# Kernel optimization log

Hardware: AMD Instinct MI355X
Metric: run time of the kernel (lower is better)

Reference implementation:

```python
import jax, jax.numpy as jnp
import numpy as np

CH = 512
RED = CH // 8  # 64


def setup_inputs() -> dict:
    key = jax.random.key(0)
    ks = jax.random.split(key, 8)
    s = 0.05
    x = jax.random.normal(ks[0], (4, CH, 64, 64), dtype=jnp.float32)
    Wq = jax.random.normal(ks[1], (RED, CH), dtype=jnp.float32) * s
    bq = jnp.zeros((RED,), dtype=jnp.float32)
    Wk = jax.random.normal(ks[2], (RED, CH), dtype=jnp.float32) * s
    bk = jnp.zeros((RED,), dtype=jnp.float32)
    Wv = jax.random.normal(ks[3], (CH, CH), dtype=jnp.float32) * s
    bv = jnp.zeros((CH,), dtype=jnp.float32)
    gamma = jnp.zeros((1,), dtype=jnp.float32)
    return {"x": x, "Wq": Wq, "bq": bq, "Wk": Wk, "bk": bk, "Wv": Wv, "bv": bv, "gamma": gamma}


def reference(x, Wq, bq, Wk, bk, Wv, bv, gamma):
    b, c, h, w = x.shape
    n = h * w
    xf = x.reshape(b, c, n)  # [b, c, n]
    # 1x1 convs == per-pixel linear over channels
    q = jnp.einsum('rc,bcn->bnr', Wq, xf) + bq[None, None, :]   # [b, n, red]
    k = jnp.einsum('rc,bcn->brn', Wk, xf) + bk[None, :, None]   # [b, red, n]
    v = jnp.einsum('oc,bcn->bon', Wv, xf) + bv[None, :, None]   # [b, c, n]
    energy = jnp.einsum('bnr,brm->bnm', q, k)                   # [b, n, n]
    attention = jax.nn.softmax(energy, axis=-1)
    # out[b,c,i] = sum_j v[b,c,j] * attention[b,i,j]
    out = jnp.einsum('bcj,bij->bci', v, attention).reshape(b, c, h, w)
    return gamma[0] * out + x
```

## Files before the change

kernel.cpp:

```cpp
#include <hip/hip_runtime.h>
#include <math.h>

#define CH 512
#define RED 64

typedef __attribute__((ext_vector_type(4))) float f32x4;
typedef long i64;

typedef const __attribute__((address_space(1))) void* gas_t;
typedef __attribute__((address_space(3))) void* las_t;

static __device__ __forceinline__ void gl16(const void* g, void* l) {
    __builtin_amdgcn_global_load_lds((gas_t)g, (las_t)l, 16, 0, 0);
}

static __device__ __forceinline__ unsigned pk4(float a, float b, float c, float d) {
    int w = __builtin_amdgcn_cvt_pk_fp8_f32(a, b, 0, false);
    w = __builtin_amdgcn_cvt_pk_fp8_f32(c, d, w, true);
    return (unsigned)w;
}
static __device__ __forceinline__ unsigned char pk1(float a) {
    return (unsigned char)(__builtin_amdgcn_cvt_pk_fp8_f32(a, a, 0, false) & 0xFF);
}

static __device__ __forceinline__ float fexp2(float v) {
#if __has_builtin(__builtin_amdgcn_exp2f)
    return __builtin_amdgcn_exp2f(v);
#else
    float r; asm("v_exp_f32 %0, %1" : "=v"(r) : "v"(v)); return r;
#endif
}

__global__ __launch_bounds__(128) void prep_w(
    const float* __restrict__ Wq, const float* __restrict__ Wk,
    const float* __restrict__ Wv, unsigned char* __restrict__ Wcat)
{
    const int r = blockIdx.x, t = threadIdx.x;
    const float* src = (r < 64) ? (Wq + (size_t)r * CH)
                     : (r < 128) ? (Wk + (size_t)(r - 64) * CH)
                                 : (Wv + (size_t)(r - 128) * CH);
    const float4 v = *(const float4*)&src[t * 4];
    *(unsigned*)&Wcat[(size_t)r * CH + t * 4] = pk4(v.x, v.y, v.z, v.w);
}

__global__ __launch_bounds__(256) void cast_xt(
    const float* __restrict__ x, unsigned char* __restrict__ xT, int n)
{
    __shared__ float sX[64][65];
    const int b = blockIdx.z, i0 = blockIdx.x * 64, c0 = blockIdx.y * 64;
    const int t = threadIdx.x;
    #pragma unroll
    for (int s = 0; s < 4; ++s) {
        const int id = s * 256 + t, c = id >> 4, seg = id & 15;
        *(float4*)&sX[c][seg * 4] = *(const float4*)&x[((size_t)b * CH + c0 + c) * n + i0 + seg * 4];
    }
    __syncthreads();
    const int i = t >> 2, cp = t & 3;
    uint4 w;
    w.x = pk4(sX[cp*16+ 0][i], sX[cp*16+ 1][i], sX[cp*16+ 2][i], sX[cp*16+ 3][i]);
    w.y = pk4(sX[cp*16+ 4][i], sX[cp*16+ 5][i], sX[cp*16+ 6][i], sX[cp*16+ 7][i]);
    w.z = pk4(sX[cp*16+ 8][i], sX[cp*16+ 9][i], sX[cp*16+10][i], sX[cp*16+11][i]);
    w.w = pk4(sX[cp*16+12][i], sX[cp*16+13][i], sX[cp*16+14][i], sX[cp*16+15][i]);
    *(uint4*)&xT[((size_t)b * n + i0 + i) * CH + c0 + cp * 16] = w;
}

__global__ __launch_bounds__(256, 4) void qkv_gemm(
    const unsigned char* __restrict__ xT, const unsigned char* __restrict__ Wcat,
    const float* __restrict__ bq, const float* __restrict__ bk,
    const float* __restrict__ bv,
    unsigned char* __restrict__ qF, unsigned char* __restrict__ kF,
    unsigned char* __restrict__ v2, int n)
{
    __shared__ char smem[20480];
    const int b = blockIdx.z, i0 = blockIdx.x * 128, o0 = blockIdx.y * 128;
    const int t = threadIdx.x, lane = t & 63;
    const int quad = lane >> 4, l16 = lane & 15;
    const int wrow = (t >> 6) & 1, wcol = t >> 7;

    f32x4 acc[4][4];
    const f32x4 zz = {0.f, 0.f, 0.f, 0.f};
    #pragma unroll
    for (int mi = 0; mi < 4; ++mi)
        #pragma unroll
        for (int ci = 0; ci < 4; ++ci) acc[mi][ci] = zz;

    const unsigned char* Ab = xT + ((size_t)b * n + i0) * CH;
    const unsigned char* Bb = Wcat + (size_t)o0 * CH;

    for (int c0 = 0; c0 < CH; c0 += 64) {
        #pragma unroll
        for (int s = 0; s < 5; ++s) {
            const int c = s * 256 + t;
            const bool isA = c < 640;
            const int tc = isA ? c : c - 640;
            const int r = tc / 5, p = (tc % 5) & 3;
            gl16((isA ? Ab : Bb) + (size_t)r * CH + c0 + p * 16,
                 smem + (isA ? 0 : 10240) + (size_t)tc * 16);
        }
        __syncthreads();
        #pragma unroll
        for (int kk = 0; kk < 64; kk += 32) {
            i64 af[4], bf[4];
            #pragma unroll
            for (int mi = 0; mi < 4; ++mi)
                af[mi] = *(const i64*)(smem + (wrow * 64 + mi * 16 + l16) * 80 + kk + quad * 8);
            #pragma unroll
            for (int ci = 0; ci < 4; ++ci)
                bf[ci] = *(const i64*)(smem + 10240 + (wcol * 64 + ci * 16 + l16) * 80 + kk + quad * 8);
            #pragma unroll
            for (int mi = 0; mi < 4; ++mi)
                #pragma unroll
                for (int ci = 0; ci < 4; ++ci)
                    acc[mi][ci] = __builtin_amdgcn_mfma_f32_16x16x32_fp8_fp8(af[mi], bf[ci], acc[mi][ci], 0, 0, 0);
        }
        __syncthreads();
    }

    float bb[4], scl[4];
    #pragma unroll
    for (int ci = 0; ci < 4; ++ci) {
        const int o = wcol * 64 + ci * 16 + l16;
        if (o0 == 0) {
            bb[ci]  = (o < 64) ? bq[o] : bk[o - 64];
            scl[ci] = (o < 64) ? 1.44269504088896f : 1.0f;
        } else {
            bb[ci]  = bv[o0 - 128 + o];
            scl[ci] = 1.0f;
        }
    }
    __syncthreads();
    unsigned char* sE = (unsigned char*)smem;
    if (o0 == 0) {
        #pragma unroll
        for (int mi = 0; mi < 4; ++mi)
            #pragma unroll
            for (int ci = 0; ci < 4; ++ci)
                #pragma unroll
                for (int r = 0; r < 4; ++r)
                    sE[(wrow*64 + mi*16 + quad*4 + r) * 144 + wcol*64 + ci*16 + l16] =
                        pk1((acc[mi][ci][r] + bb[ci]) * scl[ci]);
    } else {
        #pragma unroll
        for (int mi = 0; mi < 4; ++mi)
            #pragma unroll
            for (int ci = 0; ci < 4; ++ci)
                #pragma unroll
                for (int r = 0; r < 4; ++r)
                    sE[(wcol*64 + ci*16 + l16) * 144 + wrow*64 + mi*16 + quad*4 + r] =
                        pk1(acc[mi][ci][r] + bb[ci]);
    }
    __syncthreads();
    if (o0 == 0) {
        #pragma unroll
        for (int u = 0; u < 2; ++u) {
            const int id = u * 256 + t, i = id >> 2, p = id & 3;
            *(uint4*)&qF[((size_t)b * n + i0 + i) * RED + p * 16] = *(const uint4*)&sE[i * 144 + p * 16];
        }
        #pragma unroll
        for (int u = 0; u < 2; ++u) {
            const int id = u * 256 + t, i = id >> 2, p = id & 3;
            *(uint4*)&kF[((size_t)b * n + i0 + i) * RED + p * 16] = *(const uint4*)&sE[i * 144 + 64 + p * 16];
        }
    } else {
        #pragma unroll
        for (int u = 0; u < 4; ++u) {
            const int id = u * 256 + t, o = id >> 3, p = id & 7;
            *(uint4*)&v2[((size_t)b * CH + (o0 - 128) + o) * n + i0 + p * 16] =
                *(const uint4*)&sE[o * 144 + p * 16];
        }
    }
}

__global__ __launch_bounds__(256, 4) void rowmax(
    const unsigned char* __restrict__ qF, const unsigned char* __restrict__ kF,
    unsigned* __restrict__ mKey, int n)
{
    __shared__ char smem[20480];
    const int b = blockIdx.z, i0 = blockIdx.y * 128, j0 = blockIdx.x * 128;
    const int t = threadIdx.x, lane = t & 63;
    const int quad = lane >> 4, l16 = lane & 15;
    const int wrow = (t >> 6) & 1, wcol = t >> 7;

    const unsigned char* Qb = qF + ((size_t)b * n + i0) * RED;
    const unsigned char* Kb = kF + ((size_t)b * n + j0) * RED;
    #pragma unroll
    for (int s = 0; s < 5; ++s) {
        const int c = s * 256 + t;
        const bool isQ = c < 640;
        const int tc = isQ ? c : c - 640;
        const int r = tc / 5, p = (tc % 5) & 3;
        gl16((isQ ? Qb : Kb) + (size_t)r * RED + p * 16,
             smem + (isQ ? 0 : 10240) + (size_t)tc * 16);
    }
    __syncthreads();

    f32x4 acc[4][4];
    const f32x4 zz = {0.f, 0.f, 0.f, 0.f};
    #pragma unroll
    for (int mi = 0; mi < 4; ++mi)
        #pragma unroll
        for (int ci = 0; ci < 4; ++ci) acc[mi][ci] = zz;

    #pragma unroll
    for (int kk = 0; kk < 64; kk += 32) {
        i64 af[4], bf[4];
        #pragma unroll
        for (int mi = 0; mi < 4; ++mi)
            af[mi] = *(const i64*)(smem + (wrow * 64 + mi * 16 + l16) * 80 + kk + quad * 8);
        #pragma unroll
        for (int ci = 0; ci < 4; ++ci)
            bf[ci] = *(const i64*)(smem + 10240 + (wcol * 64 + ci * 16 + l16) * 80 + kk + quad * 8);
        #pragma unroll
        for (int mi = 0; mi < 4; ++mi)
            #pragma unroll
            for (int ci = 0; ci < 4; ++ci)
                acc[mi][ci] = __builtin_amdgcn_mfma_f32_16x16x32_fp8_fp8(af[mi], bf[ci], acc[mi][ci], 0, 0, 0);
    }

    #pragma unroll
    for (int mi = 0; mi < 4; ++mi)
        #pragma unroll
        for (int r = 0; r < 4; ++r) {
            float mx = fmaxf(fmaxf(acc[mi][0][r], acc[mi][1][r]),
                             fmaxf(acc[mi][2][r], acc[mi][3][r]));
            #pragma unroll
            for (int off = 1; off < 16; off <<= 1) mx = fmaxf(mx, __shfl_xor(mx, off));
            if (l16 == 0) {
                union { float f; unsigned u; } cv; cv.f = mx;
                const unsigned key = ((int)cv.u >= 0) ? (cv.u + 0x80000000u) : ~cv.u;
                atomicMax(&mKey[(size_t)b * n + i0 + wrow * 64 + mi * 16 + quad * 4 + r], key);
            }
        }
}

#define STGSZ 20480
#define SPOFF 40960
#define SLOFF 45056

__global__ __launch_bounds__(512, 4) void attn(
    const unsigned char* __restrict__ qF,
    const unsigned char* __restrict__ kF,
    const unsigned char* __restrict__ v2,
    const unsigned* __restrict__ mKey,
    const float* __restrict__ x, const float* __restrict__ gamma,
    float* __restrict__ y, int n)
{
    __shared__ char smem[46080];
    const int b = blockIdx.x >> 1, ch0 = (blockIdx.x & 1) * 256;
    const int i0 = blockIdx.y * 64;
    const int t = threadIdx.x, lane = t & 63, w = t >> 6;
    const int quad = lane >> 4, l16 = lane & 15;
    const int qh = w & 1, g = w >> 1;
    const int sw = (l16 >> 1) & 3;
    const int boff = (quad & 1) * 8;
    const int phalf = quad >> 1;

    const unsigned char* Qb = qF + ((size_t)b * n + i0) * RED;
    const unsigned char* Kb = kF + (size_t)b * n * RED;
    const unsigned char* Vb = v2 + ((size_t)b * CH + ch0) * n;

    {
        const int r = t >> 2, s = t & 3, gs = s ^ ((r >> 1) & 3);
        if (t < 256) {
            gl16(Qb + (size_t)r * RED + gs * 16, smem + SPOFF + (size_t)t * 16);
            gl16(Kb + (size_t)r * RED + gs * 16, smem + (size_t)t * 16);
        }
        #pragma unroll
        for (int ps = 0; ps < 2; ++ps) {
            const int id = ps * 512 + t, vr = id >> 2, vs = id & 3;
            const int vgs = vs ^ ((vr >> 1) & 3);
            gl16(Vb + (size_t)vr * n + vgs * 16, smem + 4096 + (size_t)id * 16);
        }
    }
    __syncthreads();

    i64 qreg[2][2];
    #pragma unroll
    for (int qt = 0; qt < 2; ++qt) {
        const int row = qh * 32 + qt * 16 + l16;
        #pragma unroll
        for (int kki = 0; kki < 2; ++kki) {
            const int p = (kki * 2 + phalf) ^ sw;
            qreg[qt][kki] = *(const i64*)(smem + SPOFF + row * 64 + p * 16 + boff);
        }
    }
    float mrow[2];
    #pragma unroll
    for (int qt = 0; qt < 2; ++qt) {
        const unsigned u = mKey[(size_t)b * n + i0 + qh * 32 + qt * 16 + l16];
        const unsigned bits = (u >= 0x80000000u) ? (u - 0x80000000u) : ~u;
        union { unsigned u; float f; } cv; cv.u = bits;
        mrow[qt] = cv.f;
    }

    f32x4 acc[2][4];
    const f32x4 zz = {0.f, 0.f, 0.f, 0.f};
    #pragma unroll
    for (int qt = 0; qt < 2; ++qt)
        #pragma unroll
        for (int ct = 0; ct < 4; ++ct) acc[qt][ct] = zz;
    float lacc[2] = {0.f, 0.f};

    const int nchunks = n >> 6;
    for (int c = 0; c < nchunks; ++c) {
        const int j0 = c << 6;
        char* cur = smem + (c & 1) * STGSZ;
        char* nxt = smem + ((c & 1) ^ 1) * STGSZ;

        __syncthreads();
        if (j0 + 64 < n) {
            const int jn = j0 + 64;
            const int r = t >> 2, s = t & 3, gs = s ^ ((r >> 1) & 3);
            if (t < 256)
                gl16(Kb + (size_t)(jn + r) * RED + gs * 16, nxt + (size_t)t * 16);
            #pragma unroll
            for (int ps = 0; ps < 2; ++ps) {
                const int id = ps * 512 + t, vr = id >> 2, vs = id & 3;
                const int vgs = vs ^ ((vr >> 1) & 3);
                gl16(Vb + (size_t)vr * n + jn + vgs * 16, nxt + 4096 + (size_t)id * 16);
            }
        }

        f32x4 S[2];
        S[0] = zz; S[1] = zz;
        #pragma unroll
        for (int kki = 0; kki < 2; ++kki) {
            const int p = (kki * 2 + phalf) ^ sw;
            const i64 kf = *(const i64*)(cur + (g * 16 + l16) * 64 + p * 16 + boff);
            #pragma unroll
            for (int qt = 0; qt < 2; ++qt)
                S[qt] = __builtin_amdgcn_mfma_f32_16x16x32_fp8_fp8(kf, qreg[qt][kki], S[qt], 0, 0, 0);
        }
        #pragma unroll
        for (int qt = 0; qt < 2; ++qt) {
            const float e0 = fexp2(S[qt][0] - mrow[qt]);
            const float e1 = fexp2(S[qt][1] - mrow[qt]);
            const float e2 = fexp2(S[qt][2] - mrow[qt]);
            const float e3 = fexp2(S[qt][3] - mrow[qt]);
            lacc[qt] += (e0 + e1) + (e2 + e3);
            const int qrow = qh * 32 + qt * 16 + l16;
            const int pp = g ^ sw;
            *(unsigned*)(smem + SPOFF + qrow * 64 + pp * 16 + quad * 4) = pk4(e0, e1, e2, e3);
        }
        __syncthreads();

        #pragma unroll
        for (int kki = 0; kki < 2; ++kki) {
            const int p = (kki * 2 + phalf) ^ sw;
            i64 vf[4], pf[2];
            #pragma unroll
            for (int ct = 0; ct < 4; ++ct) {
                const int row = g * 64 + ct * 16 + l16;
                vf[ct] = *(const i64*)(cur + 4096 + row * 64 + p * 16 + boff);
            }
            #pragma unroll
            for (int qt = 0; qt < 2; ++qt) {
                const int qrow = qh * 32 + qt * 16 + l16;
                pf[qt] = *(const i64*)(smem + SPOFF + qrow * 64 + p * 16 + boff);
            }
            #pragma unroll
            for (int qt = 0; qt < 2; ++qt)
                #pragma unroll
                for (int ct = 0; ct < 4; ++ct)
                    acc[qt][ct] = __builtin_amdgcn_mfma_f32_16x16x32_fp8_fp8(vf[ct], pf[qt], acc[qt][ct], 0, 0, 0);
        }
    }

    float* sL = (float*)(smem + SLOFF);
    #pragma unroll
    for (int qt = 0; qt < 2; ++qt) {
        float v = lacc[qt];
        v += __shfl_xor(v, 16);
        v += __shfl_xor(v, 32);
        lacc[qt] = v;
    }
    if (quad == 0) {
        #pragma unroll
        for (int qt = 0; qt < 2; ++qt) sL[w * 32 + qt * 16 + l16] = lacc[qt];
    }
    __syncthreads();
    float il[2];
    #pragma unroll
    for (int qt = 0; qt < 2; ++qt) {
        const int idx = qt * 16 + l16;
        il[qt] = 1.0f / (sL[qh * 32 + idx] + sL[(2 + qh) * 32 + idx] +
                         sL[(4 + qh) * 32 + idx] + sL[(6 + qh) * 32 + idx]);
    }

    const float gm = gamma[0];
    float* sT = (float*)smem;
    #pragma unroll
    for (int cr = 0; cr < 4; ++cr) {
        __syncthreads();
        if (g == cr) {
            #pragma unroll
            for (int ct = 0; ct < 4; ++ct)
                #pragma unroll
                for (int qt = 0; qt < 2; ++qt)
                    #pragma unroll
                    for (int r = 0; r < 4; ++r)
                        sT[(ct * 16 + quad * 4 + r) * 68 + qh * 32 + qt * 16 + l16] =
                            acc[qt][ct][r] * il[qt];
        }
        __syncthreads();
        const int row = t >> 3, seg = (t & 7) * 8;
        const size_t gb = ((size_t)b * CH + ch0 + cr * 64 + row) * n + i0 + seg;
        #pragma unroll
        for (int u = 0; u < 2; ++u) {
            const float4 xv = *(const float4*)&x[gb + u * 4];
            const float* op = &sT[row * 68 + seg + u * 4];
            float4 yv;
            yv.x = gm * op[0] + xv.x;
            yv.y = gm * op[1] + xv.y;
            yv.z = gm * op[2] + xv.z;
            yv.w = gm * op[3] + xv.w;
            *(float4*)&y[gb + u * 4] = yv;
        }
    }
}

extern "C" void kernel_launch(void* const* d_in, const int* in_sizes, int n_in,
                              void* d_out, int out_size, void* d_ws, size_t ws_size,
                              hipStream_t stream) {
    const float* x     = (const float*)d_in[0];
    const float* Wq    = (const float*)d_in[1];
    const float* bq    = (const float*)d_in[2];
    const float* Wk    = (const float*)d_in[3];
    const float* bk    = (const float*)d_in[4];
    const float* Wv    = (const float*)d_in[5];
    const float* bv    = (const float*)d_in[6];
    const float* gamma = (const float*)d_in[7];
    float* y = (float*)d_out;

    const int N = 64 * 64;
    const int B = in_sizes[0] / (CH * N);

    char* ws = (char*)d_ws;
    unsigned char* xT   = (unsigned char*)ws;  ws += (size_t)B * N * CH;
    unsigned char* qF   = (unsigned char*)ws;  ws += (size_t)B * N * RED;
    unsigned char* kF   = (unsigned char*)ws;  ws += (size_t)B * N * RED;
    unsigned char* v2   = (unsigned char*)ws;  ws += (size_t)B * CH * N;
    unsigned char* Wcat = (unsigned char*)ws;  ws += (size_t)640 * CH;
    unsigned* mKey      = (unsigned*)ws;

    hipMemsetAsync(mKey, 0, (size_t)B * N * 4, stream);

    prep_w<<<dim3(640), 128, 0, stream>>>(Wq, Wk, Wv, Wcat);
    cast_xt<<<dim3(N / 64, CH / 64, B), 256, 0, stream>>>(x, xT, N);
    qkv_gemm<<<dim3(N / 128, 5, B), 256, 0, stream>>>(xT, Wcat, bq, bk, bv, qF, kF, v2, N);
    rowmax<<<dim3(N / 128, N / 128, B), 256, 0, stream>>>(qF, kF, mKey, N);
    attn<<<dim3(2 * B, N / 64), 512, 0, stream>>>(qF, kF, v2, mKey, x, gamma, y, N);
}
```

Baseline: 219.3 us.

## Prefetch two chunks ahead with raw barriers and partial vmcnt waits

Restructures the attention main loop so K/V chunks are staged two iterations ahead rather than one, using raw s_barrier plus explicit lgkmcnt/vmcnt waits instead of __syncthreads, which drains all outstanding loads. Only the older chunk's loads are awaited, so the next chunk's global-to-LDS copies stay in flight across the barrier. It also raises wave priority around the MFMA blocks. The risk is subtle races if the per-wave vmcnt counts (3 vs 2) do not match the number of loads each wave issued.

```diff
diff --git a/kernel.cpp b/kernel.cpp
--- a/kernel.cpp
+++ b/kernel.cpp
@@ -29,6 +29,12 @@
 #else
     float r; asm("v_exp_f32 %0, %1" : "=v"(r) : "v"(v)); return r;
 #endif
+}
+
+static __device__ __forceinline__ void barrier_raw() {
+    asm volatile("" ::: "memory");
+    __builtin_amdgcn_s_barrier();
+    asm volatile("" ::: "memory");
 }
 
 __global__ __launch_bounds__(128) void prep_w(
@@ -259,30 +265,23 @@
     const unsigned char* Kb = kF + (size_t)b * n * RED;
     const unsigned char* Vb = v2 + ((size_t)b * CH + ch0) * n;
 
-    {
-        const int r = t >> 2, s = t & 3, gs = s ^ ((r >> 1) & 3);
-        if (t < 256) {
-            gl16(Qb + (size_t)r * RED + gs * 16, smem + SPOFF + (size_t)t * 16);
-            gl16(Kb + (size_t)r * RED + gs * 16, smem + (size_t)t * 16);
-        }
+    auto stage = [&](int jn, char* dst) {
+        const int r = t >> 2, s4 = t & 3, gs = s4 ^ ((r >> 1) & 3);
+        if (t < 256)
+            gl16(Kb + (size_t)(jn + r) * RED + gs * 16, dst + (size_t)t * 16);
         #pragma unroll
         for (int ps = 0; ps < 2; ++ps) {
             const int id = ps * 512 + t, vr = id >> 2, vs = id & 3;
             const int vgs = vs ^ ((vr >> 1) & 3);
-            gl16(Vb + (size_t)vr * n + vgs * 16, smem + 4096 + (size_t)id * 16);
-        }
-    }
-    __syncthreads();
-
-    i64 qreg[2][2];
-    #pragma unroll
-    for (int qt = 0; qt < 2; ++qt) {
-        const int row = qh * 32 + qt * 16 + l16;
-        #pragma unroll
-        for (int kki = 0; kki < 2; ++kki) {
-            const int p = (kki * 2 + phalf) ^ sw;
-            qreg[qt][kki] = *(const i64*)(smem + SPOFF + row * 64 + p * 16 + boff);
-        }
+            gl16(Vb + (size_t)vr * n + jn + vgs * 16, dst + 4096 + (size_t)id * 16);
+        }
+    };
+
+    {
+        const int r = t >> 2, s4 = t & 3, gs = s4 ^ ((r >> 1) & 3);
+        if (t < 256)
+            gl16(Qb + (size_t)r * RED + gs * 16, smem + SPOFF + (size_t)t * 16);
+        stage(0, smem);
     }
     float mrow[2];
     #pragma unroll
@@ -292,6 +291,23 @@
         union { unsigned u; float f; } cv; cv.u = bits;
         mrow[qt] = cv.f;
     }
+    __syncthreads();
+
+    i64 qreg[2][2];
+    #pragma unroll
+    for (int qt = 0; qt < 2; ++qt) {
+        const int row = qh * 32 + qt * 16 + l16;
+        #pragma unroll
+        for (int kki = 0; kki < 2; ++kki) {
+            const int p = (kki * 2 + phalf) ^ sw;
+            qreg[qt][kki] = *(const i64*)(smem + SPOFF + row * 64 + p * 16 + boff);
+        }
+    }
+    asm volatile("s_waitcnt lgkmcnt(0)" ::: "memory");
+    barrier_raw();
+
+    const int nchunks = n >> 6;
+    if (nchunks > 1) stage(64, smem + STGSZ);
 
     f32x4 acc[2][4];
     const f32x4 zz = {0.f, 0.f, 0.f, 0.f};
@@ -301,28 +317,12 @@
         for (int ct = 0; ct < 4; ++ct) acc[qt][ct] = zz;
     float lacc[2] = {0.f, 0.f};
 
-    const int nchunks = n >> 6;
     for (int c = 0; c < nchunks; ++c) {
-        const int j0 = c << 6;
         char* cur = smem + (c & 1) * STGSZ;
-        char* nxt = smem + ((c & 1) ^ 1) * STGSZ;
-
-        __syncthreads();
-        if (j0 + 64 < n) {
-            const int jn = j0 + 64;
-            const int r = t >> 2, s = t & 3, gs = s ^ ((r >> 1) & 3);
-            if (t < 256)
-                gl16(Kb + (size_t)(jn + r) * RED + gs * 16, nxt + (size_t)t * 16);
-            #pragma unroll
-            for (int ps = 0; ps < 2; ++ps) {
-                const int id = ps * 512 + t, vr = id >> 2, vs = id & 3;
-                const int vgs = vs ^ ((vr >> 1) & 3);
-                gl16(Vb + (size_t)vr * n + jn + vgs * 16, nxt + 4096 + (size_t)id * 16);
-            }
-        }
 
         f32x4 S[2];
         S[0] = zz; S[1] = zz;
+        __builtin_amdgcn_s_setprio(1);
         #pragma unroll
         for (int kki = 0; kki < 2; ++kki) {
             const int p = (kki * 2 + phalf) ^ sw;
@@ -331,6 +331,7 @@
             for (int qt = 0; qt < 2; ++qt)
                 S[qt] = __builtin_amdgcn_mfma_f32_16x16x32_fp8_fp8(kf, qreg[qt][kki], S[qt], 0, 0, 0);
         }
+        __builtin_amdgcn_s_setprio(0);
         #pragma unroll
         for (int qt = 0; qt < 2; ++qt) {
             const float e0 = fexp2(S[qt][0] - mrow[qt]);
@@ -342,8 +343,10 @@
             const int pp = g ^ sw;
             *(unsigned*)(smem + SPOFF + qrow * 64 + pp * 16 + quad * 4) = pk4(e0, e1, e2, e3);
         }
-        __syncthreads();
-
+        asm volatile("s_waitcnt lgkmcnt(0)" ::: "memory");
+        barrier_raw();
+
+        __builtin_amdgcn_s_setprio(1);
         #pragma unroll
         for (int kki = 0; kki < 2; ++kki) {
             const int p = (kki * 2 + phalf) ^ sw;
@@ -363,6 +366,22 @@
                 #pragma unroll
                 for (int ct = 0; ct < 4; ++ct)
                     acc[qt][ct] = __builtin_amdgcn_mfma_f32_16x16x32_fp8_fp8(vf[ct], pf[qt], acc[qt][ct], 0, 0, 0);
+        }
+        __builtin_amdgcn_s_setprio(0);
+
+        asm volatile("s_waitcnt lgkmcnt(0)" ::: "memory");
+        barrier_raw();
+
+        if (c + 2 < nchunks) {
+            stage((c + 2) << 6, cur);
+            if (w < 4) asm volatile("s_waitcnt vmcnt(3)" ::: "memory");
+            else       asm volatile("s_waitcnt vmcnt(2)" ::: "memory");
+            __builtin_amdgcn_sched_barrier(0);
+            barrier_raw();
+        } else if (c + 1 < nchunks) {
+            asm volatile("s_waitcnt vmcnt(0)" ::: "memory");
+            __builtin_amdgcn_sched_barrier(0);
+            barrier_raw();
         }
     }
 
```

Result: slower. 225.5 us (+2.8%).

## Restructure attention main loop with explicit double-buffer pipeline and raw barriers

Applied to the files above, without the earlier changes.

Rewrites the attention chunk loop as a macro unrolled by two over fixed smem buffers. It precomputes swizzled LDS addresses and advances global pointers incrementally. Prefetches are issued after compute, and the loop waits on them with explicit vmcnt counts and raw s_barrier instead of __syncthreads. It also uses s_setprio around the MFMA sections. The aim is to cut barrier and address overhead and to overlap loads with compute, at the cost of fragile manual waitcnt bookkeeping.

```diff
diff --git a/kernel.cpp b/kernel.cpp
--- a/kernel.cpp
+++ b/kernel.cpp
@@ -29,6 +29,12 @@
 #else
     float r; asm("v_exp_f32 %0, %1" : "=v"(r) : "v"(v)); return r;
 #endif
+}
+
+static __device__ __forceinline__ void barrier_raw() {
+    asm volatile("" ::: "memory");
+    __builtin_amdgcn_s_barrier();
+    asm volatile("" ::: "memory");
 }
 
 __global__ __launch_bounds__(128) void prep_w(
@@ -236,6 +242,65 @@
 #define STGSZ 20480
 #define SPOFF 40960
 #define SLOFF 45056
+
+#define CHUNK(BASE, cc) do {                                                  \
+    f32x4 S_[2] = {zz, zz};                                                   \
+    __builtin_amdgcn_s_setprio(1);                                            \
+    {                                                                         \
+        const i64 kf0 = *(const i64*)(smem + (BASE) + fA);                    \
+        const i64 kf1 = *(const i64*)(smem + (BASE) + (fA ^ 32));             \
+        S_[0] = __builtin_amdgcn_mfma_f32_16x16x32_fp8_fp8(kf0, qreg[0][0], S_[0], 0, 0, 0); \
+        S_[1] = __builtin_amdgcn_mfma_f32_16x16x32_fp8_fp8(kf0, qreg[1][0], S_[1], 0, 0, 0); \
+        S_[0] = __builtin_amdgcn_mfma_f32_16x16x32_fp8_fp8(kf1, qreg[0][1], S_[0], 0, 0, 0); \
+        S_[1] = __builtin_amdgcn_mfma_f32_16x16x32_fp8_fp8(kf1, qreg[1][1], S_[1], 0, 0, 0); \
+    }                                                                         \
+    __builtin_amdgcn_s_setprio(0);                                            \
+    _Pragma("unroll")                                                         \
+    for (int qt = 0; qt < 2; ++qt) {                                          \
+        const float e0 = fexp2(S_[qt][0] - mrow[qt]);                         \
+        const float e1 = fexp2(S_[qt][1] - mrow[qt]);                         \
+        const float e2 = fexp2(S_[qt][2] - mrow[qt]);                         \
+        const float e3 = fexp2(S_[qt][3] - mrow[qt]);                         \
+        lacc[qt] += (e0 + e1) + (e2 + e3);                                    \
+        *(unsigned*)(smem + pwA + qt * 1024) = pk4(e0, e1, e2, e3);           \
+    }                                                                         \
+    asm volatile("s_waitcnt lgkmcnt(0)" ::: "memory");                        \
+    barrier_raw();         \
+    __builtin_amdgcn_s_setprio(1);                                            \
+    _Pragma("unroll")                                                         \
+    for (int kki = 0; kki < 2; ++kki) {                                       \
+        const int kx = kki << 5;                                              \
+        i64 vf_[4], pf_[2];                                                   \
+        _Pragma("unroll")                                                     \
+        for (int ct = 0; ct < 4; ++ct)                                        \
+            vf_[ct] = *(const i64*)(smem + (BASE) + (vA ^ kx) + ct * 1024);   \
+        _Pragma("unroll")                                                     \
+        for (int qt = 0; qt < 2; ++qt)                                        \
+            pf_[qt] = *(const i64*)(smem + (pA ^ kx) + qt * 1024);            \
+        _Pragma("unroll")                                                     \
+        for (int qt = 0; qt < 2; ++qt)                                        \
+            _Pragma("unroll")                                                 \
+            for (int ct = 0; ct < 4; ++ct)                                    \
+                acc[qt][ct] = __builtin_amdgcn_mfma_f32_16x16x32_fp8_fp8(vf_[ct], pf_[qt], acc[qt][ct], 0, 0, 0); \
+    }                                                                         \
+    __builtin_amdgcn_s_setprio(0);                                            \
+    asm volatile("s_waitcnt lgkmcnt(0)" ::: "memory");                        \
+    barrier_raw();                        \
+    if ((cc) + 2 < nchunks) {                                                 \
+        if (t < 256) gl16(kP, smem + (BASE) + kDstOff);                       \
+        gl16(vP0, smem + (BASE) + vDstOff0);                                  \
+        gl16(vP1, smem + (BASE) + vDstOff1);                                  \
+        kP += 4096; vP0 += 64; vP1 += 64;                                     \
+        if (w < 4) asm volatile("s_waitcnt vmcnt(3)" ::: "memory");           \
+        else       asm volatile("s_waitcnt vmcnt(2)" ::: "memory");           \
+        __builtin_amdgcn_sched_barrier(0);                                    \
+        barrier_raw();                        \
+    } else if ((cc) + 1 < nchunks) {                                          \
+        asm volatile("s_waitcnt vmcnt(0)" ::: "memory");                      \
+        __builtin_amdgcn_sched_barrier(0);                                    \
+        barrier_raw();                                                        \
+    }                                                                         \
+} while (0)
 
 __global__ __launch_bounds__(512, 4) void attn(
     const unsigned char* __restrict__ qF,
@@ -254,36 +319,32 @@
     const int sw = (l16 >> 1) & 3;
     const int boff = (quad & 1) * 8;
     const int phalf = quad >> 1;
+    const int p0 = phalf ^ sw;
+
+    const int fA  = (g * 16 + l16) * 64 + p0 * 16 + boff;
+    const int vA  = 4096 + (g * 64 + l16) * 64 + p0 * 16 + boff;
+    const int pA  = SPOFF + (qh * 32 + l16) * 64 + p0 * 16 + boff;
+    const int pwA = SPOFF + (qh * 32 + l16) * 64 + (g ^ sw) * 16 + quad * 4;
 
     const unsigned char* Qb = qF + ((size_t)b * n + i0) * RED;
     const unsigned char* Kb = kF + (size_t)b * n * RED;
     const unsigned char* Vb = v2 + ((size_t)b * CH + ch0) * n;
 
-    {
-        const int r = t >> 2, s = t & 3, gs = s ^ ((r >> 1) & 3);
-        if (t < 256) {
-            gl16(Qb + (size_t)r * RED + gs * 16, smem + SPOFF + (size_t)t * 16);
-            gl16(Kb + (size_t)r * RED + gs * 16, smem + (size_t)t * 16);
-        }
-        #pragma unroll
-        for (int ps = 0; ps < 2; ++ps) {
-            const int id = ps * 512 + t, vr = id >> 2, vs = id & 3;
-            const int vgs = vs ^ ((vr >> 1) & 3);
-            gl16(Vb + (size_t)vr * n + vgs * 16, smem + 4096 + (size_t)id * 16);
-        }
-    }
-    __syncthreads();
-
-    i64 qreg[2][2];
-    #pragma unroll
-    for (int qt = 0; qt < 2; ++qt) {
-        const int row = qh * 32 + qt * 16 + l16;
-        #pragma unroll
-        for (int kki = 0; kki < 2; ++kki) {
-            const int p = (kki * 2 + phalf) ^ sw;
-            qreg[qt][kki] = *(const i64*)(smem + SPOFF + row * 64 + p * 16 + boff);
-        }
-    }
+    const int r = t >> 2, s4 = t & 3, gs = s4 ^ ((r >> 1) & 3);
+    const int kDstOff  = t * 16;
+    const int vDstOff0 = 4096 + t * 16;
+    const int vDstOff1 = 12288 + t * 16;
+    const size_t vHalf = (size_t)128 * n;
+    const unsigned char* kSrc0 = Kb + (size_t)r * RED + gs * 16;
+    const unsigned char* vSrc0 = Vb + (size_t)r * n + gs * 16;
+
+    if (t < 256) {
+        gl16(Qb + (size_t)r * RED + gs * 16, smem + SPOFF + kDstOff);
+        gl16(kSrc0, smem + kDstOff);
+    }
+    gl16(vSrc0, smem + vDstOff0);
+    gl16(vSrc0 + vHalf, smem + vDstOff1);
+
     float mrow[2];
     #pragma unroll
     for (int qt = 0; qt < 2; ++qt) {
@@ -292,6 +353,27 @@
         union { unsigned u; float f; } cv; cv.u = bits;
         mrow[qt] = cv.f;
     }
+    __syncthreads();
+
+    i64 qreg[2][2];
+    #pragma unroll
+    for (int qt = 0; qt < 2; ++qt) {
+        #pragma unroll
+        for (int kki = 0; kki < 2; ++kki)
+            qreg[qt][kki] = *(const i64*)(smem + ((pA ^ (kki << 5)) + qt * 1024));
+    }
+    asm volatile("s_waitcnt lgkmcnt(0)" ::: "memory");
+    barrier_raw();
+
+    const int nchunks = n >> 6;
+    if (nchunks > 1) {
+        if (t < 256) gl16(kSrc0 + 4096, smem + STGSZ + kDstOff);
+        gl16(vSrc0 + 64, smem + STGSZ + vDstOff0);
+        gl16(vSrc0 + vHalf + 64, smem + STGSZ + vDstOff1);
+    }
+    const unsigned char* kP  = kSrc0 + 8192;
+    const unsigned char* vP0 = vSrc0 + 128;
+    const unsigned char* vP1 = vSrc0 + vHalf + 128;
 
     f32x4 acc[2][4];
     const f32x4 zz = {0.f, 0.f, 0.f, 0.f};
@@ -301,69 +383,9 @@
         for (int ct = 0; ct < 4; ++ct) acc[qt][ct] = zz;
     float lacc[2] = {0.f, 0.f};
 
-    const int nchunks = n >> 6;
-    for (int c = 0; c < nchunks; ++c) {
-        const int j0 = c << 6;
-        char* cur = smem + (c & 1) * STGSZ;
-        char* nxt = smem + ((c & 1) ^ 1) * STGSZ;
-
-        __syncthreads();
-        if (j0 + 64 < n) {
-            const int jn = j0 + 64;
-            const int r = t >> 2, s = t & 3, gs = s ^ ((r >> 1) & 3);
-            if (t < 256)
-                gl16(Kb + (size_t)(jn + r) * RED + gs * 16, nxt + (size_t)t * 16);
-            #pragma unroll
-            for (int ps = 0; ps < 2; ++ps) {
-                const int id = ps * 512 + t, vr = id >> 2, vs = id & 3;
-                const int vgs = vs ^ ((vr >> 1) & 3);
-                gl16(Vb + (size_t)vr * n + jn + vgs * 16, nxt + 4096 + (size_t)id * 16);
-            }
-        }
-
-        f32x4 S[2];
-        S[0] = zz; S[1] = zz;
-        #pragma unroll
-        for (int kki = 0; kki < 2; ++kki) {
-            const int p = (kki * 2 + phalf) ^ sw;
-            const i64 kf = *(const i64*)(cur + (g * 16 + l16) * 64 + p * 16 + boff);
-            #pragma unroll
-            for (int qt = 0; qt < 2; ++qt)
-                S[qt] = __builtin_amdgcn_mfma_f32_16x16x32_fp8_fp8(kf, qreg[qt][kki], S[qt], 0, 0, 0);
-        }
-        #pragma unroll
-        for (int qt = 0; qt < 2; ++qt) {
-            const float e0 = fexp2(S[qt][0] - mrow[qt]);
-            const float e1 = fexp2(S[qt][1] - mrow[qt]);
-            const float e2 = fexp2(S[qt][2] - mrow[qt]);
-            const float e3 = fexp2(S[qt][3] - mrow[qt]);
-            lacc[qt] += (e0 + e1) + (e2 + e3);
-            const int qrow = qh * 32 + qt * 16 + l16;
-            const int pp = g ^ sw;
-            *(unsigned*)(smem + SPOFF + qrow * 64 + pp * 16 + quad * 4) = pk4(e0, e1, e2, e3);
-        }
-        __syncthreads();
-
-        #pragma unroll
-        for (int kki = 0; kki < 2; ++kki) {
-            const int p = (kki * 2 + phalf) ^ sw;
-            i64 vf[4], pf[2];
-            #pragma unroll
-            for (int ct = 0; ct < 4; ++ct) {
-                const int row = g * 64 + ct * 16 + l16;
-                vf[ct] = *(const i64*)(cur + 4096 + row * 64 + p * 16 + boff);
-            }
-            #pragma unroll
-            for (int qt = 0; qt < 2; ++qt) {
-                const int qrow = qh * 32 + qt * 16 + l16;
-                pf[qt] = *(const i64*)(smem + SPOFF + qrow * 64 + p * 16 + boff);
-            }
-            #pragma unroll
-            for (int qt = 0; qt < 2; ++qt)
-                #pragma unroll
-                for (int ct = 0; ct < 4; ++ct)
-                    acc[qt][ct] = __builtin_amdgcn_mfma_f32_16x16x32_fp8_fp8(vf[ct], pf[qt], acc[qt][ct], 0, 0, 0);
-        }
+    for (int c = 0; c < nchunks; c += 2) {
+        CHUNK(0, c);
+        CHUNK(STGSZ, c + 1);
     }
 
     float* sL = (float*)(smem + SLOFF);
@@ -398,9 +420,9 @@
                 #pragma unroll
                 for (int qt = 0; qt < 2; ++qt)
                     #pragma unroll
-                    for (int r = 0; r < 4; ++r)
-                        sT[(ct * 16 + quad * 4 + r) * 68 + qh * 32 + qt * 16 + l16] =
-                            acc[qt][ct][r] * il[qt];
+                    for (int rr = 0; rr < 4; ++rr)
+                        sT[(ct * 16 + quad * 4 + rr) * 68 + qh * 32 + qt * 16 + l16] =
+                            acc[qt][ct][rr] * il[qt];
         }
         __syncthreads();
         const int row = t >> 3, seg = (t & 7) * 8;
```

New measurement: 228.3 us. 4.1% more time.
